# Performance work log

Measured on AMD Instinct MI355X. Metric: run time of the kernel, lower is better.

Reference implementation:

```python
import jax, jax.numpy as jnp
import numpy as np

IN_FEATURES_A = 256
IN_FEATURES_B = 256


def setup_inputs() -> dict:
    key = jax.random.key(0)
    # x: [2, batch, features]; x[0] -> x_a, x[1] -> x_b
    x = jax.random.normal(key, (2, 2048, 256), dtype=jnp.float32)
    return {"x": x}


def reference(x) -> jnp.ndarray:
    # Split and truncate exactly like the torch module
    x_a = x[0][:, :IN_FEATURES_A]  # [B, A]
    x_b = x[1][:, :IN_FEATURES_B]  # [B, Kb]
    bsz = x_a.shape[0]
    # torch.kron of two 1-D vectors == flattened outer product (a-major order)
    y = jnp.einsum("ba,bk->bak", x_a, x_b).reshape(bsz, IN_FEATURES_A * IN_FEATURES_B)
    return jax.nn.softmax(y, axis=1)
```

## Files before the change

### kernel.cpp

```cpp
#include <hip/hip_runtime.h>


constexpr int FA   = 256;
constexpr int FB   = 256;
constexpr int ROWS = 2048;
constexpr float LOG2E = 1.4426950408889634f;

typedef float f32x4 __attribute__((ext_vector_type(4)));

__global__ __launch_bounds__(256) void krone_reduce_kernel(
    const float* __restrict__ x, float* __restrict__ Cbuf) {
  const int row = blockIdx.x;
  const int tid = threadIdx.x;

  const float* __restrict__ xa = x + (size_t)row * FA;
  const float* __restrict__ xb = x + (size_t)ROWS * FA + (size_t)row * FB;

  __shared__ float sa[FA];
  __shared__ float wred[4][4];
  __shared__ float wsum[4];

  const float a = xa[tid];
  const float b = xb[tid];
  sa[tid] = a;

  float maxa = a, mina = a, maxb = b, minb = b;
#pragma unroll
  for (int off = 32; off > 0; off >>= 1) {
    maxa = fmaxf(maxa, __shfl_xor(maxa, off));
    mina = fminf(mina, __shfl_xor(mina, off));
    maxb = fmaxf(maxb, __shfl_xor(maxb, off));
    minb = fminf(minb, __shfl_xor(minb, off));
  }
  const int wid = tid >> 6;
  if ((tid & 63) == 0) {
    wred[wid][0] = maxa; wred[wid][1] = mina;
    wred[wid][2] = maxb; wred[wid][3] = minb;
  }
  __syncthreads();
  const float MA = fmaxf(fmaxf(wred[0][0], wred[1][0]), fmaxf(wred[2][0], wred[3][0]));
  const float mA = fminf(fminf(wred[0][1], wred[1][1]), fminf(wred[2][1], wred[3][1]));
  const float MB = fmaxf(fmaxf(wred[0][2], wred[1][2]), fmaxf(wred[2][2], wred[3][2]));
  const float mB = fminf(fminf(wred[0][3], wred[1][3]), fminf(wred[2][3], wred[3][3]));
  const float M = fmaxf(fmaxf(MA * MB, MA * mB), fmaxf(mA * MB, mA * mB));
  const float mM2 = -M * LOG2E;

  const float bs = b * LOG2E;
  float s0 = 0.f, s1 = 0.f, s2 = 0.f, s3 = 0.f;
#pragma unroll 4
  for (int i = 0; i < FA; i += 4) {
    s0 += __builtin_amdgcn_exp2f(fmaf(sa[i + 0], bs, mM2));
    s1 += __builtin_amdgcn_exp2f(fmaf(sa[i + 1], bs, mM2));
    s2 += __builtin_amdgcn_exp2f(fmaf(sa[i + 2], bs, mM2));
    s3 += __builtin_amdgcn_exp2f(fmaf(sa[i + 3], bs, mM2));
  }
  float s = (s0 + s1) + (s2 + s3);
#pragma unroll
  for (int off = 32; off > 0; off >>= 1) s += __shfl_xor(s, off);
  if ((tid & 63) == 0) wsum[wid] = s;
  __syncthreads();
  if (tid == 0) {
    const float sum = (wsum[0] + wsum[1]) + (wsum[2] + wsum[3]);
    Cbuf[row] = mM2 - __builtin_amdgcn_logf(sum);
  }
}

__global__ __launch_bounds__(256) void krone_store_kernel(
    const float* __restrict__ x, const float* __restrict__ Cbuf,
    float* __restrict__ out) {
  const int row = blockIdx.x;
  const int tid = threadIdx.x;
  const int wid = tid >> 6;
  const int lane = tid & 63;

  const float* __restrict__ xa = x + (size_t)row * FA;
  const float* __restrict__ xb = x + (size_t)ROWS * FA + (size_t)row * FB;

  const float aval = xa[wid * 64 + lane];
  const int j = lane * 4;
  f32x4 b4 = *reinterpret_cast<const f32x4*>(&xb[j]);
  b4 *= LOG2E;
  const float C = Cbuf[row];

  float* __restrict__ oseg = out + (size_t)row * (FA * FB) + wid * (64 * FB);
#pragma unroll 8
  for (int it = 0; it < 64; ++it) {
    const float av = __shfl(aval, it);
    f32x4 v;
    v.x = __builtin_amdgcn_exp2f(fmaf(av, b4.x, C));
    v.y = __builtin_amdgcn_exp2f(fmaf(av, b4.y, C));
    v.z = __builtin_amdgcn_exp2f(fmaf(av, b4.z, C));
    v.w = __builtin_amdgcn_exp2f(fmaf(av, b4.w, C));
    __builtin_nontemporal_store(v, reinterpret_cast<f32x4*>(&oseg[it * FB + j]));
  }
}

__global__ __launch_bounds__(256) void krone_fused_kernel(
    const float* __restrict__ x, float* __restrict__ out) {
  const int row = blockIdx.x;
  const int tid = threadIdx.x;
  const float* __restrict__ xa = x + (size_t)row * FA;
  const float* __restrict__ xb = x + (size_t)ROWS * FA + (size_t)row * FB;
  __shared__ float sa[FA];
  __shared__ float sb[FB];
  __shared__ float wred[4][4];
  __shared__ float wsum[4];
  const float a = xa[tid];
  const float b = xb[tid];
  sa[tid] = a; sb[tid] = b;
  float maxa = a, mina = a, maxb = b, minb = b;
#pragma unroll
  for (int off = 32; off > 0; off >>= 1) {
    maxa = fmaxf(maxa, __shfl_xor(maxa, off));
    mina = fminf(mina, __shfl_xor(mina, off));
    maxb = fmaxf(maxb, __shfl_xor(maxb, off));
    minb = fminf(minb, __shfl_xor(minb, off));
  }
  const int wid = tid >> 6;
  if ((tid & 63) == 0) {
    wred[wid][0] = maxa; wred[wid][1] = mina;
    wred[wid][2] = maxb; wred[wid][3] = minb;
  }
  __syncthreads();
  const float MA = fmaxf(fmaxf(wred[0][0], wred[1][0]), fmaxf(wred[2][0], wred[3][0]));
  const float mA = fminf(fminf(wred[0][1], wred[1][1]), fminf(wred[2][1], wred[3][1]));
  const float MB = fmaxf(fmaxf(wred[0][2], wred[1][2]), fmaxf(wred[2][2], wred[3][2]));
  const float mB = fminf(fminf(wred[0][3], wred[1][3]), fminf(wred[2][3], wred[3][3]));
  const float M = fmaxf(fmaxf(MA * MB, MA * mB), fmaxf(mA * MB, mA * mB));
  const float mM2 = -M * LOG2E;
  const float bs = b * LOG2E;
  float s0 = 0.f, s1 = 0.f, s2 = 0.f, s3 = 0.f;
#pragma unroll 4
  for (int i = 0; i < FA; i += 4) {
    s0 += __builtin_amdgcn_exp2f(fmaf(sa[i + 0], bs, mM2));
    s1 += __builtin_amdgcn_exp2f(fmaf(sa[i + 1], bs, mM2));
    s2 += __builtin_amdgcn_exp2f(fmaf(sa[i + 2], bs, mM2));
    s3 += __builtin_amdgcn_exp2f(fmaf(sa[i + 3], bs, mM2));
  }
  float s = (s0 + s1) + (s2 + s3);
#pragma unroll
  for (int off = 32; off > 0; off >>= 1) s += __shfl_xor(s, off);
  if ((tid & 63) == 0) wsum[wid] = s;
  __syncthreads();
  const float sum = (wsum[0] + wsum[1]) + (wsum[2] + wsum[3]);
  const float C = mM2 - __builtin_amdgcn_logf(sum);
  float* __restrict__ orow = out + (size_t)row * (FA * FB);
  const int lane = tid & 63;
  const int j = lane * 4;
  f32x4 b4 = *reinterpret_cast<const f32x4*>(&sb[j]);
  b4 *= LOG2E;
  float* __restrict__ oseg = orow + wid * (64 * FB);
#pragma unroll 8
  for (int it = 0; it < 64; ++it) {
    const float av = sa[wid * 64 + it];
    f32x4 v;
    v.x = __builtin_amdgcn_exp2f(fmaf(av, b4.x, C));
    v.y = __builtin_amdgcn_exp2f(fmaf(av, b4.y, C));
    v.z = __builtin_amdgcn_exp2f(fmaf(av, b4.z, C));
    v.w = __builtin_amdgcn_exp2f(fmaf(av, b4.w, C));
    __builtin_nontemporal_store(v, reinterpret_cast<f32x4*>(&oseg[it * FB + j]));
  }
}

extern "C" void kernel_launch(void* const* d_in, const int* in_sizes, int n_in,
                              void* d_out, int out_size, void* d_ws, size_t ws_size,
                              hipStream_t stream) {
  const float* x = (const float*)d_in[0];
  float* out = (float*)d_out;
  if (ws_size >= ROWS * sizeof(float)) {
    float* Cbuf = (float*)d_ws;
    krone_reduce_kernel<<<ROWS, 256, 0, stream>>>(x, Cbuf);
    krone_store_kernel<<<ROWS, 256, 0, stream>>>(x, Cbuf, out);
  } else {
    krone_fused_kernel<<<ROWS, 256, 0, stream>>>(x, out);
  }
}
```

Measured before the change: 116.7 us.

## Replace per-row store kernel with persistent grid-stride sweep and prefetch

The per-row store kernel becomes a persistent sweep: 2048 blocks of 4 waves each walk global 256-element output chunks in grid-stride order, prefetching the next chunk's a value, row constant and b vector while computing the current one. Nontemporal stores are replaced with regular stores in both the sweep and fused kernels. The aim is to smooth the write stream across the GPU and hide input-load latency, at the cost of one redundant global load of a and b per chunk and losing the cache-bypass hint on a 512MB write.

```diff
diff --git a/kernel.cpp b/kernel.cpp
--- a/kernel.cpp
+++ b/kernel.cpp
@@ -4,6 +4,8 @@
 constexpr int FA   = 256;
 constexpr int FB   = 256;
 constexpr int ROWS = 2048;
+constexpr int NCHUNK = ROWS * FA;
+constexpr int NWAVE  = 8192;
 constexpr float LOG2E = 1.4426950408889634f;
 
 typedef float f32x4 __attribute__((ext_vector_type(4)));
@@ -65,33 +67,41 @@
   }
 }
 
-__global__ __launch_bounds__(256) void krone_store_kernel(
+__global__ __launch_bounds__(256) void krone_sweep_kernel(
     const float* __restrict__ x, const float* __restrict__ Cbuf,
     float* __restrict__ out) {
-  const int row = blockIdx.x;
-  const int tid = threadIdx.x;
-  const int wid = tid >> 6;
-  const int lane = tid & 63;
+  const int tid   = threadIdx.x;
+  const int lane  = tid & 63;
+  const int gwave = (blockIdx.x << 2) | (tid >> 6);
+  const float* __restrict__ xb = x + (size_t)ROWS * FA;
 
-  const float* __restrict__ xa = x + (size_t)row * FA;
-  const float* __restrict__ xb = x + (size_t)ROWS * FA + (size_t)row * FB;
+  int g   = gwave;
+  int row = g >> 8, c = g & 255;
+  float av = x[row * FA + c];
+  float C  = Cbuf[row];
+  f32x4 b4 = *reinterpret_cast<const f32x4*>(&xb[row * FB + lane * 4]);
 
-  const float aval = xa[wid * 64 + lane];
-  const int j = lane * 4;
-  f32x4 b4 = *reinterpret_cast<const f32x4*>(&xb[j]);
-  b4 *= LOG2E;
-  const float C = Cbuf[row];
+#pragma unroll 2
+  for (int t = 0; t < NCHUNK / NWAVE; ++t) {
+    const int gn = g + NWAVE;
+    float avn = 0.f, Cn = 0.f;
+    f32x4 b4n = {0.f, 0.f, 0.f, 0.f};
+    if (gn < NCHUNK) {
+      const int rown = gn >> 8, cn = gn & 255;
+      avn = x[rown * FA + cn];
+      Cn  = Cbuf[rown];
+      b4n = *reinterpret_cast<const f32x4*>(&xb[rown * FB + lane * 4]);
+    }
 
-  float* __restrict__ oseg = out + (size_t)row * (FA * FB) + wid * (64 * FB);
-#pragma unroll 8
-  for (int it = 0; it < 64; ++it) {
-    const float av = __shfl(aval, it);
+    const float avl = av * LOG2E;
     f32x4 v;
-    v.x = __builtin_amdgcn_exp2f(fmaf(av, b4.x, C));
-    v.y = __builtin_amdgcn_exp2f(fmaf(av, b4.y, C));
-    v.z = __builtin_amdgcn_exp2f(fmaf(av, b4.z, C));
-    v.w = __builtin_amdgcn_exp2f(fmaf(av, b4.w, C));
-    __builtin_nontemporal_store(v, reinterpret_cast<f32x4*>(&oseg[it * FB + j]));
+    v.x = __builtin_amdgcn_exp2f(fmaf(avl, b4.x, C));
+    v.y = __builtin_amdgcn_exp2f(fmaf(avl, b4.y, C));
+    v.z = __builtin_amdgcn_exp2f(fmaf(avl, b4.z, C));
+    v.w = __builtin_amdgcn_exp2f(fmaf(avl, b4.w, C));
+    *reinterpret_cast<f32x4*>(&out[(size_t)g * 256 + lane * 4]) = v;
+
+    g = gn; av = avn; C = Cn; b4 = b4n;
   }
 }
 
@@ -158,7 +168,7 @@
     v.y = __builtin_amdgcn_exp2f(fmaf(av, b4.y, C));
     v.z = __builtin_amdgcn_exp2f(fmaf(av, b4.z, C));
     v.w = __builtin_amdgcn_exp2f(fmaf(av, b4.w, C));
-    __builtin_nontemporal_store(v, reinterpret_cast<f32x4*>(&oseg[it * FB + j]));
+    *reinterpret_cast<f32x4*>(&oseg[it * FB + j]) = v;
   }
 }
 
@@ -170,7 +180,7 @@
   if (ws_size >= ROWS * sizeof(float)) {
     float* Cbuf = (float*)d_ws;
     krone_reduce_kernel<<<ROWS, 256, 0, stream>>>(x, Cbuf);
-    krone_store_kernel<<<ROWS, 256, 0, stream>>>(x, Cbuf, out);
+    krone_sweep_kernel<<<NWAVE / 4, 256, 0, stream>>>(x, Cbuf, out);
   } else {
     krone_fused_kernel<<<ROWS, 256, 0, stream>>>(x, out);
   }
```

Result: slower. 132.6 us (+13.6%).

## Assign whole rows to single wavefronts in store kernel with fewer blocks

Applied to the files above, without the earlier changes.

The store kernel now launches 256 blocks instead of 2048. Each wavefront handles two complete rows, writing all four 64-row segments of each output row itself instead of splitting a row across four waves. This reduces block-launch overhead and gives each wave long sequential write streams. The cost is fewer concurrent blocks (256 over the CUs), which could limit memory-level parallelism. The fallback fused kernel also switches from nontemporal to regular stores.

```diff
diff --git a/kernel.cpp b/kernel.cpp
--- a/kernel.cpp
+++ b/kernel.cpp
@@ -65,33 +65,50 @@
   }
 }
 
-__global__ __launch_bounds__(256) void krone_store_kernel(
+__global__ __launch_bounds__(256) void krone_stream_kernel(
     const float* __restrict__ x, const float* __restrict__ Cbuf,
     float* __restrict__ out) {
-  const int row = blockIdx.x;
-  const int tid = threadIdx.x;
-  const int wid = tid >> 6;
+  const int tid  = threadIdx.x;
+  const int wid  = tid >> 6;
   const int lane = tid & 63;
+  const int gw   = (blockIdx.x << 2) | wid;
 
-  const float* __restrict__ xa = x + (size_t)row * FA;
-  const float* __restrict__ xb = x + (size_t)ROWS * FA + (size_t)row * FB;
+#pragma unroll
+  for (int r = 0; r < 2; ++r) {
+    const int row = gw * 2 + r;
+    const float* __restrict__ xa = x + (size_t)row * FA;
+    const float* __restrict__ xb = x + (size_t)ROWS * FA + (size_t)row * FB;
 
-  const float aval = xa[wid * 64 + lane];
-  const int j = lane * 4;
-  f32x4 b4 = *reinterpret_cast<const f32x4*>(&xb[j]);
-  b4 *= LOG2E;
-  const float C = Cbuf[row];
+    f32x4 b4 = *reinterpret_cast<const f32x4*>(&xb[lane * 4]);
+    b4 *= LOG2E;
+    const float C = Cbuf[row];
+    const float a0 = xa[lane];
+    const float a1 = xa[64 + lane];
+    const float a2 = xa[128 + lane];
+    const float a3 = xa[192 + lane];
 
-  float* __restrict__ oseg = out + (size_t)row * (FA * FB) + wid * (64 * FB);
-#pragma unroll 8
-  for (int it = 0; it < 64; ++it) {
-    const float av = __shfl(aval, it);
-    f32x4 v;
-    v.x = __builtin_amdgcn_exp2f(fmaf(av, b4.x, C));
-    v.y = __builtin_amdgcn_exp2f(fmaf(av, b4.y, C));
-    v.z = __builtin_amdgcn_exp2f(fmaf(av, b4.z, C));
-    v.w = __builtin_amdgcn_exp2f(fmaf(av, b4.w, C));
-    __builtin_nontemporal_store(v, reinterpret_cast<f32x4*>(&oseg[it * FB + j]));
+    float* __restrict__ orow = out + (size_t)row * (FA * FB);
+
+#define KS_BLK(I, AREG)                                                       \
+    {                                                                         \
+      float* __restrict__ oseg = orow + (I) * (64 * FB);                      \
+      _Pragma("unroll 8")                                                     \
+      for (int k = 0; k < 64; ++k) {                                          \
+        const float av = __shfl(AREG, k);         \
+        f32x4 v;                                                              \
+        v.x = __builtin_amdgcn_exp2f(fmaf(av, b4.x, C));                      \
+        v.y = __builtin_amdgcn_exp2f(fmaf(av, b4.y, C));                      \
+        v.z = __builtin_amdgcn_exp2f(fmaf(av, b4.z, C));                      \
+        v.w = __builtin_amdgcn_exp2f(fmaf(av, b4.w, C));                      \
+        __builtin_nontemporal_store(                                          \
+            v, reinterpret_cast<f32x4*>(&oseg[k * FB + lane * 4]));           \
+      }                                                                       \
+    }
+    KS_BLK(0, a0)
+    KS_BLK(1, a1)
+    KS_BLK(2, a2)
+    KS_BLK(3, a3)
+#undef KS_BLK
   }
 }
 
@@ -158,7 +175,7 @@
     v.y = __builtin_amdgcn_exp2f(fmaf(av, b4.y, C));
     v.z = __builtin_amdgcn_exp2f(fmaf(av, b4.z, C));
     v.w = __builtin_amdgcn_exp2f(fmaf(av, b4.w, C));
-    __builtin_nontemporal_store(v, reinterpret_cast<f32x4*>(&oseg[it * FB + j]));
+    *reinterpret_cast<f32x4*>(&oseg[it * FB + j]) = v;
   }
 }
 
@@ -170,7 +187,7 @@
   if (ws_size >= ROWS * sizeof(float)) {
     float* Cbuf = (float*)d_ws;
     krone_reduce_kernel<<<ROWS, 256, 0, stream>>>(x, Cbuf);
-    krone_store_kernel<<<ROWS, 256, 0, stream>>>(x, Cbuf, out);
+    krone_stream_kernel<<<256, 256, 0, stream>>>(x, Cbuf, out);
   } else {
     krone_fused_kernel<<<ROWS, 256, 0, stream>>>(x, out);
   }
```

New measurement: 127.7 us. 9.4% more time.
